# Optimization experiments

Measured on AMD Instinct MI355X. Metric: run time of the kernel, lower is better.

The kernel has to match this reference:

```python
import jax, jax.numpy as jnp
from jax import lax
import numpy as np

# Problem dims (see init_kwargs)
B, CIN, H, W = 4, 128, 128, 128
COUT, K, STRIDE, PAD, DIL, GROUPS, OG = 128, 3, 1, 1, 1, 1, 2


def setup_inputs() -> dict:
    key = jax.random.key(0)
    k0, k1, k2 = jax.random.split(key, 3)
    x = jax.random.normal(k0, (B, CIN, H, W), dtype=jnp.float32)
    off_ch = 3 * OG * K * K  # with_mask=True -> scale=3 (dy, dx, mask)
    # Small random offset-conv weights so offsets are non-trivial (zero-init would degenerate to plain conv)
    w_off = jax.random.normal(k1, (off_ch, CIN, K, K), dtype=jnp.float32) * 0.01
    b_off = jnp.zeros((off_ch,), jnp.float32)
    stdv = 1.0 / np.sqrt(CIN * K * K)
    weight = jax.random.uniform(k2, (COUT, CIN // GROUPS, K, K), jnp.float32, -stdv, stdv)
    bias = jnp.zeros((COUT,), jnp.float32)
    return {"x": x, "w_off": w_off, "b_off": b_off, "weight": weight, "bias": bias}


def _deform_conv2d(x, offset, mask, weight, bias):
    # x: [B,C,H,W]; offset: [B,2*OG*K2,Ho,Wo]; mask: [B,OG*K2,Ho,Wo]
    Bn, C, Hn, Wn = x.shape
    O = weight.shape[0]
    K2 = K * K
    Ho = (Hn + 2 * PAD - DIL * (K - 1) - 1) // STRIDE + 1
    Wo = (Wn + 2 * PAD - DIL * (K - 1) - 1) // STRIDE + 1
    # torchvision layout: per offset group, per kernel point, (dy, dx) interleaved
    off = offset.reshape(Bn, OG, K2, 2, Ho, Wo)
    kg = (jnp.arange(K) * DIL).astype(x.dtype)
    kyf = jnp.repeat(kg, K)  # [K2] kernel row offset, k2 = i*K + j
    kxf = jnp.tile(kg, K)    # [K2] kernel col offset
    base_y = (jnp.arange(Ho) * STRIDE - PAD).astype(x.dtype)
    base_x = (jnp.arange(Wo) * STRIDE - PAD).astype(x.dtype)
    # sampling coords: [B,OG,K2,Ho,Wo]
    sy = base_y[None, None, None, :, None] + kyf[None, None, :, None, None] + off[:, :, :, 0]
    sx = base_x[None, None, None, None, :] + kxf[None, None, :, None, None] + off[:, :, :, 1]
    y0f = jnp.floor(sy)
    x0f = jnp.floor(sx)
    ly = sy - y0f  # bilinear fractional weights
    lx = sx - x0f
    y0 = y0f.astype(jnp.int32)
    x0 = x0f.astype(jnp.int32)
    Cg = C // OG
    xg = x.reshape(Bn, OG, Cg, Hn * Wn)

    def gather(iy, ix):
        # zero-padding semantics: out-of-range corners contribute 0
        valid = ((iy >= 0) & (iy < Hn) & (ix >= 0) & (ix < Wn)).astype(x.dtype)
        idx = (jnp.clip(iy, 0, Hn - 1) * Wn + jnp.clip(ix, 0, Wn - 1)).reshape(Bn, OG, 1, -1)
        v = jnp.take_along_axis(xg, idx, axis=3).reshape(Bn, OG, Cg, K2, Ho, Wo)
        return v * valid[:, :, None]

    v00 = gather(y0, x0)
    v01 = gather(y0, x0 + 1)
    v10 = gather(y0 + 1, x0)
    v11 = gather(y0 + 1, x0 + 1)
    wy = ly[:, :, None]  # broadcast over channel dim
    wx = lx[:, :, None]
    val = (v00 * (1 - wy) * (1 - wx) + v01 * (1 - wy) * wx
           + v10 * wy * (1 - wx) + v11 * wy * wx)
    # modulated DCNv2: multiply sampled values by sigmoid mask
    val = val * mask.reshape(Bn, OG, 1, K2, Ho, Wo)
    # im2col GEMM: cols [B,G,(C/G)*K2,Ho*Wo] x weight [G,O/G,(C/G)*K2]
    cols = val.reshape(Bn, GROUPS, (C // GROUPS) * K2, Ho * Wo)
    wg = weight.reshape(GROUPS, O // GROUPS, (C // GROUPS) * K2)
    out = jnp.einsum('gok,bgkn->bgon', wg, cols).reshape(Bn, O, Ho, Wo)
    return out + bias[None, :, None, None]


def reference(x, w_off, b_off, weight, bias):
    off_out = lax.conv_general_dilated(
        x, w_off, (STRIDE, STRIDE), [(PAD, PAD), (PAD, PAD)],
        rhs_dilation=(DIL, DIL), dimension_numbers=('NCHW', 'OIHW', 'NCHW')
    ) + b_off[None, :, None, None]
    oh, ow, m = jnp.split(off_out, 3, axis=1)
    offset = jnp.concatenate([oh, ow], axis=1)
    mask = jax.nn.sigmoid(m)
    return _deform_conv2d(x, offset, mask, weight, bias)
```

## Files before the change

kernel.cpp:

```cpp
#include <hip/hip_runtime.h>
#include <math.h>

#define NB 4
#define NC 128
#define NH 128
#define NW 128
#define NHW (NH*NW)
#define NCOUT 128

#define SY_OFF 0
#define SX_OFF 1179648
#define MK_OFF 2359296
#define WOFF_OFF 3538944
#define WMAIN_OFF 3580416
#define XT_OFF 3663360

typedef short short8 __attribute__((ext_vector_type(8)));
typedef float f32x4 __attribute__((ext_vector_type(4)));

__device__ inline short f2bf(float f) {
    unsigned u = __float_as_uint(f);
    u = (u + 0x7FFFu + ((u >> 16) & 1u)) >> 16;
    return (short)u;
}
__device__ inline unsigned pack2(float lo, float hi) {
    unsigned r;
    asm("v_cvt_pk_bf16_f32 %0, %1, %2" : "=v"(r) : "v"(lo), "v"(hi));
    return r;
}
__device__ inline float bflo(unsigned u) { return __uint_as_float(u << 16); }
__device__ inline float bfhi(unsigned u) { return __uint_as_float(u & 0xffff0000u); }

__device__ inline void gload_lds16(const void* g, void* l) {
    __builtin_amdgcn_global_load_lds(
        (const __attribute__((address_space(1))) unsigned int*)g,
        (__attribute__((address_space(3))) unsigned int*)l, 16, 0, 0);
}

__global__ void wtrans_kernel(const float* __restrict__ w_off,
                              const float* __restrict__ weight,
                              float* __restrict__ ws)
{
    int i = blockIdx.x * 256 + threadIdx.x;
    if (i < 36*2304) {
        int s = i / 2304, rem = i - s*2304;
        int row = rem / 36, c = rem - row*36;
        int chunk = s / 9, k2 = s - 9*chunk;
        float v = (row < 54 && c < 32) ? w_off[(row*NC + chunk*32 + c)*9 + k2] : 0.f;
        ((short*)(ws + WOFF_OFF))[i] = f2bf(v);
    } else if (i < 36*2304 + 36*4608) {
        int j = i - 36*2304;
        int s = j / 4608, rem = j - s*4608;
        int row = rem / 36, c = rem - row*36;
        int chunk = s / 9, k2 = s - 9*chunk;
        float v = (c < 32) ? weight[(row*NC + chunk*32 + c)*9 + k2] : 0.f;
        ((short*)(ws + WMAIN_OFF))[j] = f2bf(v);
    }
}

__global__ __launch_bounds__(256) void xtrans_kernel(
    const float* __restrict__ x, float* __restrict__ ws)
{
    short* xT = (short*)(ws + XT_OFF);
    const int bid = blockIdx.x;
    const int ys = bid & 15, cg = (bid >> 4) & 15, b = bid >> 8;
    const int col = threadIdx.x & 127, rr = threadIdx.x >> 7;
    const float* xb = x + ((long)(b*NC + cg*8))*NHW;
#pragma unroll
    for (int yy = 0; yy < 4; ++yy) {
        const int y = ys*8 + yy*2 + rr;
        const float* p = xb + y*NW + col;
        float v[8];
#pragma unroll
        for (int q = 0; q < 8; ++q) v[q] = p[q*NHW];
        uint4 u = make_uint4(pack2(v[0],v[1]), pack2(v[2],v[3]),
                             pack2(v[4],v[5]), pack2(v[6],v[7]));
        *(uint4*)&xT[(((long)(b*16+cg)*NH + y)*NW + col)*8] = u;
    }
}

__global__ __launch_bounds__(512, 4) void offconv_kernel(
    float* __restrict__ ws, const float* __restrict__ b_off)
{
    __shared__ short wslab[2][2304];
    int bid = blockIdx.x;
    bid = (bid & 7) * 64 + (bid >> 3);
    const int b   = bid >> 7;
    const int ho  = bid & 127;
    const int tid = threadIdx.x;
    const int lane = tid & 63;
    const int wid = tid >> 6;
    const int n = lane & 15, g = lane >> 4;
    const int px = wid*16 + n;
    const short* woff = (const short*)(ws + WOFF_OFF);
    const char*  xTb  = (const char*)((const short*)(ws + XT_OFF) + (long)b*16*NHW*8);

    f32x4 acc[4];
#pragma unroll
    for (int rf = 0; rf < 4; ++rf) acc[rf] = (f32x4){0.f,0.f,0.f,0.f};

    auto DMA = [&](int it, int buf) {
        if (tid < 288) gload_lds16(woff + it*2304 + tid*8, &wslab[buf][tid*8]);
    };
    auto LOADB = [&](int it) -> short8 {
        const int chunk = it/9, k2 = it - 9*chunk;
        const int y = ho + k2/3 - 1, xc = px + (k2%3) - 1;
        short8 bf = (short8){0,0,0,0,0,0,0,0};
        if ((unsigned)y < NH && (unsigned)xc < NW)
            bf = *(const short8*)(xTb + ((long)(chunk*4 + g)*NHW + y*NW + xc)*16);
        return bf;
    };

    DMA(0, 0);
    short8 bcur = LOADB(0);
    __syncthreads();

#pragma unroll 1
    for (int it = 0; it < 36; ++it) {
        const int cur = it & 1, nxt = cur ^ 1;
        short8 bnext;
        if (it < 35) { DMA(it+1, nxt); bnext = LOADB(it+1); }
        __builtin_amdgcn_sched_barrier(0);
#pragma unroll
        for (int rf = 0; rf < 4; ++rf) {
            short8 af = *(const short8*)&wslab[cur][(rf*16 + n)*36 + 8*g];
            acc[rf] = __builtin_amdgcn_mfma_f32_16x16x32_bf16(af, bcur, acc[rf], 0,0,0);
        }
        __syncthreads();
        bcur = bnext;
    }

#pragma unroll
    for (int rf = 0; rf < 4; ++rf) {
#pragma unroll
        for (int r = 0; r < 4; ++r) {
            int cout = 16*rf + 4*g + r;
            if (cout >= 54) continue;
            float v = acc[rf][r] + b_off[cout];
            if (cout < 36) {
                int og = cout / 18, rem = cout - 18*og;
                int k2c = rem >> 1, d = cout & 1;
                float base = d ? (float)(px - 1 + (k2c % 3))
                              : (float)(ho - 1 + (k2c / 3));
                ws[(d ? SX_OFF : SY_OFF) + (((b*2+og)*9 + k2c)*NHW) + ho*NW + px] = v + base;
            } else {
                int cc = cout - 36;
                int og = cc / 9, k2c = cc - 9*og;
                ws[MK_OFF + (((b*2+og)*9 + k2c)*NHW) + ho*NW + px] = 1.f/(1.f+expf(-v));
            }
        }
    }
}

__global__ __launch_bounds__(512, 4) void deform_kernel(
    const float* __restrict__ ws_c, float* __restrict__ ws,
    const float* __restrict__ bias, float* __restrict__ out)
{
    __shared__ int4   pI[9][128];
    __shared__ float4 pW[9][128];
    __shared__ short  vals[2][128][40];
    __shared__ short  wslab[2][4608];

    int bid = blockIdx.x;
    bid = (bid & 7) * 64 + (bid >> 3);
    const int b   = bid >> 7;
    const int ho  = bid & 127;
    const int tid = threadIdx.x;
    const int lane = tid & 63;
    const int wid = tid >> 6;
    const int n = lane & 15, g = lane >> 4;
    const int ch  = wid & 1;
    const int pxq = wid >> 1;
    const int sp  = tid & 127;
    const int sub = tid >> 7;
    const short* wmn = (const short*)(ws + WMAIN_OFF);
    const char*  xTb = (const char*)((const short*)(ws + XT_OFF) + (long)b*16*NHW*8);

    f32x4 acc[4][2];
#pragma unroll
    for (int rf = 0; rf < 4; ++rf) {
        acc[rf][0] = (f32x4){0.f,0.f,0.f,0.f};
        acc[rf][1] = (f32x4){0.f,0.f,0.f,0.f};
    }

    auto DMA = [&](int slabIdx, int buf) {
        const short* src = wmn + slabIdx*4608;
        gload_lds16(src + tid*8, &wslab[buf][tid*8]);
        if (tid < 64) gload_lds16(src + 4096 + tid*8, &wslab[buf][4096 + tid*8]);
    };

    auto FIN = [&](const uint4& A, const uint4& Bc, const uint4& Cc, const uint4& D,
                   const float4& Wv, int buf) {
        uint4 u; unsigned* up = (unsigned*)&u;
        const unsigned* a = (const unsigned*)&A;
        const unsigned* bq = (const unsigned*)&Bc;
        const unsigned* c = (const unsigned*)&Cc;
        const unsigned* d = (const unsigned*)&D;
#pragma unroll
        for (int e = 0; e < 4; ++e) {
            float lo = Wv.x*bflo(a[e]) + Wv.y*bflo(bq[e]) + Wv.z*bflo(c[e]) + Wv.w*bflo(d[e]);
            float hi = Wv.x*bfhi(a[e]) + Wv.y*bfhi(bq[e]) + Wv.z*bfhi(c[e]) + Wv.w*bfhi(d[e]);
            up[e] = pack2(lo, hi);
        }
        *(uint4*)&vals[buf][sp][sub*8] = u;
    };

    DMA(0, 0);

#pragma unroll 1
    for (int og = 0; og < 2; ++og) {
        if (og) __syncthreads();
        for (int e = tid; e < 1152; e += 512) {
            const int k2 = e >> 7, px = e & 127;
            const int sidx = (((b*2+og)*9 + k2)*NHW) + ho*NW + px;
            const float sy = ws[SY_OFF + sidx];
            const float sx = ws[SX_OFF + sidx];
            const float m  = ws[MK_OFF + sidx];
            const float y0f = floorf(sy), x0f = floorf(sx);
            const float ly = sy - y0f, lx = sx - x0f;
            const int y0 = (int)y0f, x0i = (int)x0f;
            const int y1 = y0 + 1, x1 = x0i + 1;
            const bool vy0 = (unsigned)y0 < NH, vy1 = (unsigned)y1 < NH;
            const bool vx0 = (unsigned)x0i < NW, vx1 = (unsigned)x1 < NW;
            const int cy0 = min(max(y0,0),NH-1), cy1 = min(max(y1,0),NH-1);
            const int cx0 = min(max(x0i,0),NW-1), cx1 = min(max(x1,0),NW-1);
            pI[k2][px] = make_int4((cy0*NW + cx0)*16, (cy0*NW + cx1)*16,
                                   (cy1*NW + cx0)*16, (cy1*NW + cx1)*16);
            pW[k2][px] = make_float4(
                (vy0 && vx0) ? (1.f-ly)*(1.f-lx)*m : 0.f,
                (vy0 && vx1) ? (1.f-ly)*lx*m       : 0.f,
                (vy1 && vx0) ? ly*(1.f-lx)*m       : 0.f,
                (vy1 && vx1) ? ly*lx*m             : 0.f);
        }
        __syncthreads();

        const int it0 = og*18;

        {
            const int chunk = it0/9, k2n = it0 - 9*chunk;
            const int4  I  = pI[k2n][sp];
            const float4 Wv = pW[k2n][sp];
            const char* xp = xTb + (long)(chunk*4 + sub)*(NHW*16);
            uint4 A  = *(const uint4*)(xp + I.x);
            uint4 Bc = *(const uint4*)(xp + I.y);
            uint4 Cc = *(const uint4*)(xp + I.z);
            uint4 D  = *(const uint4*)(xp + I.w);
            FIN(A, Bc, Cc, D, Wv, 0);
        }
        __syncthreads();

#pragma unroll 1
        for (int it = it0; it < it0 + 18; ++it) {
            const int cur = it & 1, nxt = cur ^ 1;
            const bool pre = (it < it0 + 17);

            uint4 A, Bc, Cc, D;
            float4 Wv;
            if (pre) {
                const int itn = it + 1;
                const int chunk = itn/9, k2n = itn - 9*chunk;
                const int4 I = pI[k2n][sp];
                Wv = pW[k2n][sp];
                const char* xp = xTb + (long)(chunk*4 + sub)*(NHW*16);
                A  = *(const uint4*)(xp + I.x);
                Bc = *(const uint4*)(xp + I.y);
                Cc = *(const uint4*)(xp + I.z);
                D  = *(const uint4*)(xp + I.w);
                DMA(itn, nxt);
            } else if (og == 0) {
                DMA(18, nxt);
            }
            __builtin_amdgcn_sched_barrier(0);

            {
                short8 bf0 = *(const short8*)&vals[cur][pxq*32 + n][8*g];
                short8 bf1 = *(const short8*)&vals[cur][pxq*32 + 16 + n][8*g];
#pragma unroll
                for (int rf = 0; rf < 4; ++rf) {
                    short8 af = *(const short8*)&wslab[cur][(ch*64 + rf*16 + n)*36 + 8*g];
                    acc[rf][0] = __builtin_amdgcn_mfma_f32_16x16x32_bf16(af, bf0, acc[rf][0], 0,0,0);
                    acc[rf][1] = __builtin_amdgcn_mfma_f32_16x16x32_bf16(af, bf1, acc[rf][1], 0,0,0);
                }
            }
            __builtin_amdgcn_sched_barrier(0);

            if (pre) FIN(A, Bc, Cc, D, Wv, nxt);
            __syncthreads();
        }
    }

#pragma unroll
    for (int rf = 0; rf < 4; ++rf) {
#pragma unroll
        for (int pxb = 0; pxb < 2; ++pxb) {
            const int px = pxq*32 + pxb*16 + n;
#pragma unroll
            for (int r = 0; r < 4; ++r) {
                const int cout = ch*64 + rf*16 + 4*g + r;
                out[((b*NCOUT + cout)*NH + ho)*NW + px] = acc[rf][pxb][r] + bias[cout];
            }
        }
    }
}

extern "C" void kernel_launch(void* const* d_in, const int* in_sizes, int n_in,
                              void* d_out, int out_size, void* d_ws, size_t ws_size,
                              hipStream_t stream)
{
    const float* x      = (const float*)d_in[0];
    const float* w_off  = (const float*)d_in[1];
    const float* b_off  = (const float*)d_in[2];
    const float* weight = (const float*)d_in[3];
    const float* bias   = (const float*)d_in[4];
    float* out = (float*)d_out;
    float* ws  = (float*)d_ws;

    hipLaunchKernelGGL(wtrans_kernel, dim3(972), dim3(256), 0, stream,
                       w_off, weight, ws);
    hipLaunchKernelGGL(xtrans_kernel, dim3(1024), dim3(256), 0, stream,
                       x, ws);
    hipLaunchKernelGGL(offconv_kernel, dim3(NB*NH), dim3(512), 0, stream,
                       ws, b_off);
    hipLaunchKernelGGL(deform_kernel, dim3(NB*NH), dim3(512), 0, stream,
                       ws, ws, bias, out);
}
```

Baseline: 90.62 us.

## Split deform blocks to half-rows and load weight fragments directly into registers

The deform kernel now uses 256-thread blocks that each cover half an output row, doubling the grid. The LDS weight slab and its async DMA are removed; each wave loads its bf16 weight A-fragments straight from global memory into registers, prefetched one iteration ahead, and the weight layout drops its 36-wide padding to a dense 32. Sampling indices are stored as short4 to shrink LDS use. The aim is lower LDS footprint and higher occupancy, at the cost of redundant global weight loads per wave and duplicated per-pixel setup work across more blocks.

```diff
diff --git a/kernel.cpp b/kernel.cpp
--- a/kernel.cpp
+++ b/kernel.cpp
@@ -48,13 +48,12 @@
         int chunk = s / 9, k2 = s - 9*chunk;
         float v = (row < 54 && c < 32) ? w_off[(row*NC + chunk*32 + c)*9 + k2] : 0.f;
         ((short*)(ws + WOFF_OFF))[i] = f2bf(v);
-    } else if (i < 36*2304 + 36*4608) {
+    } else if (i < 36*2304 + 36*4096) {
         int j = i - 36*2304;
-        int s = j / 4608, rem = j - s*4608;
-        int row = rem / 36, c = rem - row*36;
+        int s = j >> 12, rem = j & 4095;
+        int row = rem >> 5, c = rem & 31;
         int chunk = s / 9, k2 = s - 9*chunk;
-        float v = (c < 32) ? weight[(row*NC + chunk*32 + c)*9 + k2] : 0.f;
-        ((short*)(ws + WMAIN_OFF))[j] = f2bf(v);
+        ((short*)(ws + WMAIN_OFF))[j] = f2bf(weight[(row*NC + chunk*32 + c)*9 + k2]);
     }
 }
 
@@ -152,27 +151,27 @@
     }
 }
 
-__global__ __launch_bounds__(512, 4) void deform_kernel(
+__global__ __launch_bounds__(256, 4) void deform_kernel(
     const float* __restrict__ ws_c, float* __restrict__ ws,
     const float* __restrict__ bias, float* __restrict__ out)
 {
-    __shared__ int4   pI[9][128];
-    __shared__ float4 pW[9][128];
-    __shared__ short  vals[2][128][40];
-    __shared__ short  wslab[2][4608];
+    __shared__ short4 pI[9][64];
+    __shared__ float4 pW[9][64];
+    __shared__ short  vals[2][64][40];
 
     int bid = blockIdx.x;
-    bid = (bid & 7) * 64 + (bid >> 3);
-    const int b   = bid >> 7;
-    const int ho  = bid & 127;
+    bid = (bid & 7) * 128 + (bid >> 3);
+    const int b   = bid >> 8;
+    const int ho  = (bid >> 1) & 127;
+    const int wb  = (bid & 1) * 64;
     const int tid = threadIdx.x;
     const int lane = tid & 63;
     const int wid = tid >> 6;
     const int n = lane & 15, g = lane >> 4;
     const int ch  = wid & 1;
-    const int pxq = wid >> 1;
-    const int sp  = tid & 127;
-    const int sub = tid >> 7;
+    const int pxh = wid >> 1;
+    const int sp  = tid & 63;
+    const int sub = tid >> 6;
     const short* wmn = (const short*)(ws + WMAIN_OFF);
     const char*  xTb = (const char*)((const short*)(ws + XT_OFF) + (long)b*16*NHW*8);
 
@@ -182,12 +181,6 @@
         acc[rf][0] = (f32x4){0.f,0.f,0.f,0.f};
         acc[rf][1] = (f32x4){0.f,0.f,0.f,0.f};
     }
-
-    auto DMA = [&](int slabIdx, int buf) {
-        const short* src = wmn + slabIdx*4608;
-        gload_lds16(src + tid*8, &wslab[buf][tid*8]);
-        if (tid < 64) gload_lds16(src + 4096 + tid*8, &wslab[buf][4096 + tid*8]);
-    };
 
     auto FIN = [&](const uint4& A, const uint4& Bc, const uint4& Cc, const uint4& D,
                    const float4& Wv, int buf) {
@@ -205,14 +198,17 @@
         *(uint4*)&vals[buf][sp][sub*8] = u;
     };
 
-    DMA(0, 0);
+    short8 acur0, acur1, acur2, acur3;
+    #define LOADA(dst, it, rf) \
+        dst = *(const short8*)(wmn + (it)*4096 + (ch*64 + (rf)*16 + n)*32 + 8*g)
 
 #pragma unroll 1
     for (int og = 0; og < 2; ++og) {
+        const int it0 = og*18;
         if (og) __syncthreads();
-        for (int e = tid; e < 1152; e += 512) {
-            const int k2 = e >> 7, px = e & 127;
-            const int sidx = (((b*2+og)*9 + k2)*NHW) + ho*NW + px;
+        for (int e = tid; e < 576; e += 256) {
+            const int k2 = e >> 6, px = e & 63;
+            const int sidx = (((b*2+og)*9 + k2)*NHW) + ho*NW + wb + px;
             const float sy = ws[SY_OFF + sidx];
             const float sx = ws[SX_OFF + sidx];
             const float m  = ws[MK_OFF + sidx];
@@ -224,8 +220,8 @@
             const bool vx0 = (unsigned)x0i < NW, vx1 = (unsigned)x1 < NW;
             const int cy0 = min(max(y0,0),NH-1), cy1 = min(max(y1,0),NH-1);
             const int cx0 = min(max(x0i,0),NW-1), cx1 = min(max(x1,0),NW-1);
-            pI[k2][px] = make_int4((cy0*NW + cx0)*16, (cy0*NW + cx1)*16,
-                                   (cy1*NW + cx0)*16, (cy1*NW + cx1)*16);
+            pI[k2][px] = make_short4((short)(cy0*NW + cx0), (short)(cy0*NW + cx1),
+                                     (short)(cy1*NW + cx0), (short)(cy1*NW + cx1));
             pW[k2][px] = make_float4(
                 (vy0 && vx0) ? (1.f-ly)*(1.f-lx)*m : 0.f,
                 (vy0 && vx1) ? (1.f-ly)*lx*m       : 0.f,
@@ -234,17 +230,19 @@
         }
         __syncthreads();
 
-        const int it0 = og*18;
-
+        if (og == 0) {
+            LOADA(acur0, 0, 0); LOADA(acur1, 0, 1);
+            LOADA(acur2, 0, 2); LOADA(acur3, 0, 3);
+        }
         {
             const int chunk = it0/9, k2n = it0 - 9*chunk;
-            const int4  I  = pI[k2n][sp];
+            const short4 I = pI[k2n][sp];
             const float4 Wv = pW[k2n][sp];
             const char* xp = xTb + (long)(chunk*4 + sub)*(NHW*16);
-            uint4 A  = *(const uint4*)(xp + I.x);
-            uint4 Bc = *(const uint4*)(xp + I.y);
-            uint4 Cc = *(const uint4*)(xp + I.z);
-            uint4 D  = *(const uint4*)(xp + I.w);
+            uint4 A  = *(const uint4*)(xp + (((int)I.x) << 4));
+            uint4 Bc = *(const uint4*)(xp + (((int)I.y) << 4));
+            uint4 Cc = *(const uint4*)(xp + (((int)I.z) << 4));
+            uint4 D  = *(const uint4*)(xp + (((int)I.w) << 4));
             FIN(A, Bc, Cc, D, Wv, 0);
         }
         __syncthreads();
@@ -254,38 +252,43 @@
             const int cur = it & 1, nxt = cur ^ 1;
             const bool pre = (it < it0 + 17);
 
+            short8 anxt0, anxt1, anxt2, anxt3;
             uint4 A, Bc, Cc, D;
             float4 Wv;
+            if (it < 35) {
+                LOADA(anxt0, it+1, 0); LOADA(anxt1, it+1, 1);
+                LOADA(anxt2, it+1, 2); LOADA(anxt3, it+1, 3);
+            }
             if (pre) {
                 const int itn = it + 1;
                 const int chunk = itn/9, k2n = itn - 9*chunk;
-                const int4 I = pI[k2n][sp];
+                const short4 I = pI[k2n][sp];
                 Wv = pW[k2n][sp];
                 const char* xp = xTb + (long)(chunk*4 + sub)*(NHW*16);
-                A  = *(const uint4*)(xp + I.x);
-                Bc = *(const uint4*)(xp + I.y);
-                Cc = *(const uint4*)(xp + I.z);
-                D  = *(const uint4*)(xp + I.w);
-                DMA(itn, nxt);
-            } else if (og == 0) {
-                DMA(18, nxt);
+                A  = *(const uint4*)(xp + (((int)I.x) << 4));
+                Bc = *(const uint4*)(xp + (((int)I.y) << 4));
+                Cc = *(const uint4*)(xp + (((int)I.z) << 4));
+                D  = *(const uint4*)(xp + (((int)I.w) << 4));
             }
             __builtin_amdgcn_sched_barrier(0);
 
             {
-                short8 bf0 = *(const short8*)&vals[cur][pxq*32 + n][8*g];
-                short8 bf1 = *(const short8*)&vals[cur][pxq*32 + 16 + n][8*g];
-#pragma unroll
-                for (int rf = 0; rf < 4; ++rf) {
-                    short8 af = *(const short8*)&wslab[cur][(ch*64 + rf*16 + n)*36 + 8*g];
-                    acc[rf][0] = __builtin_amdgcn_mfma_f32_16x16x32_bf16(af, bf0, acc[rf][0], 0,0,0);
-                    acc[rf][1] = __builtin_amdgcn_mfma_f32_16x16x32_bf16(af, bf1, acc[rf][1], 0,0,0);
-                }
+                short8 bf0 = *(const short8*)&vals[cur][pxh*32 + n][8*g];
+                short8 bf1 = *(const short8*)&vals[cur][pxh*32 + 16 + n][8*g];
+                acc[0][0] = __builtin_amdgcn_mfma_f32_16x16x32_bf16(acur0, bf0, acc[0][0], 0,0,0);
+                acc[0][1] = __builtin_amdgcn_mfma_f32_16x16x32_bf16(acur0, bf1, acc[0][1], 0,0,0);
+                acc[1][0] = __builtin_amdgcn_mfma_f32_16x16x32_bf16(acur1, bf0, acc[1][0], 0,0,0);
+                acc[1][1] = __builtin_amdgcn_mfma_f32_16x16x32_bf16(acur1, bf1, acc[1][1], 0,0,0);
+                acc[2][0] = __builtin_amdgcn_mfma_f32_16x16x32_bf16(acur2, bf0, acc[2][0], 0,0,0);
+                acc[2][1] = __builtin_amdgcn_mfma_f32_16x16x32_bf16(acur2, bf1, acc[2][1], 0,0,0);
+                acc[3][0] = __builtin_amdgcn_mfma_f32_16x16x32_bf16(acur3, bf0, acc[3][0], 0,0,0);
+                acc[3][1] = __builtin_amdgcn_mfma_f32_16x16x32_bf16(acur3, bf1, acc[3][1], 0,0,0);
             }
             __builtin_amdgcn_sched_barrier(0);
 
             if (pre) FIN(A, Bc, Cc, D, Wv, nxt);
             __syncthreads();
+            acur0 = anxt0; acur1 = anxt1; acur2 = anxt2; acur3 = anxt3;
         }
     }
 
@@ -293,7 +296,7 @@
     for (int rf = 0; rf < 4; ++rf) {
 #pragma unroll
         for (int pxb = 0; pxb < 2; ++pxb) {
-            const int px = pxq*32 + pxb*16 + n;
+            const int px = wb + pxh*32 + pxb*16 + n;
 #pragma unroll
             for (int r = 0; r < 4; ++r) {
                 const int cout = ch*64 + rf*16 + 4*g + r;
@@ -301,6 +304,7 @@
             }
         }
     }
+    #undef LOADA
 }
 
 extern "C" void kernel_launch(void* const* d_in, const int* in_sizes, int n_in,
@@ -315,12 +319,12 @@
     float* out = (float*)d_out;
     float* ws  = (float*)d_ws;
 
-    hipLaunchKernelGGL(wtrans_kernel, dim3(972), dim3(256), 0, stream,
+    hipLaunchKernelGGL(wtrans_kernel, dim3(900), dim3(256), 0, stream,
                        w_off, weight, ws);
     hipLaunchKernelGGL(xtrans_kernel, dim3(1024), dim3(256), 0, stream,
                        x, ws);
     hipLaunchKernelGGL(offconv_kernel, dim3(NB*NH), dim3(512), 0, stream,
                        ws, b_off);
-    hipLaunchKernelGGL(deform_kernel, dim3(NB*NH), dim3(512), 0, stream,
+    hipLaunchKernelGGL(deform_kernel, dim3(NB*NH*2), dim3(256), 0, stream,
                        ws, ws, bias, out);
 }
```

Measured after the change: 106.4 us. 1.17x slower.

## Deepen gather prefetch to two iterations and merge offset-group sampling setup

Applied to the files above, without the earlier changes.

Sampling indices and bilinear weights for both offset groups are now computed once up front into LDS. Indices are stored as 16-bit shorts and weights as packed fp16, which shrinks LDS enough to hold 18 rows. The main loop is unrolled by two with ping-pong register buffers, so the global gathers run two iterations ahead of the MFMA work. Barriers use explicit vmcnt/lgkmcnt waits instead of __syncthreads. This removes the mid-kernel stall between offset groups and hides gather latency, at the cost of more registers and fp16 rounding of the weights.

```diff
diff --git a/kernel.cpp b/kernel.cpp
--- a/kernel.cpp
+++ b/kernel.cpp
@@ -30,7 +30,14 @@
 }
 __device__ inline float bflo(unsigned u) { return __uint_as_float(u << 16); }
 __device__ inline float bfhi(unsigned u) { return __uint_as_float(u & 0xffff0000u); }
-
+__device__ inline unsigned pkf16(float a, float b) {
+    auto h = __builtin_amdgcn_cvt_pkrtz(a, b);
+    unsigned r; __builtin_memcpy(&r, &h, 4); return r;
+}
+__device__ inline float f16f(unsigned s) {
+    unsigned short us = (unsigned short)s;
+    __fp16 h; __builtin_memcpy(&h, &us, 2); return (float)h;
+}
 __device__ inline void gload_lds16(const void* g, void* l) {
     __builtin_amdgcn_global_load_lds(
         (const __attribute__((address_space(1))) unsigned int*)g,
@@ -156,8 +163,8 @@
     const float* __restrict__ ws_c, float* __restrict__ ws,
     const float* __restrict__ bias, float* __restrict__ out)
 {
-    __shared__ int4   pI[9][128];
-    __shared__ float4 pW[9][128];
+    __shared__ short4 pI[18][128];
+    __shared__ uint2  pWp[18][128];
     __shared__ short  vals[2][128][40];
     __shared__ short  wslab[2][4608];
 
@@ -188,18 +195,30 @@
         gload_lds16(src + tid*8, &wslab[buf][tid*8]);
         if (tid < 64) gload_lds16(src + 4096 + tid*8, &wslab[buf][4096 + tid*8]);
     };
-
-    auto FIN = [&](const uint4& A, const uint4& Bc, const uint4& Cc, const uint4& D,
-                   const float4& Wv, int buf) {
+    auto GLOAD = [&](int j, uint4* G) {
+        const int chunk = j/9;
+        const int row = (j/18)*9 + (j%9);
+        const short4 I = pI[row][sp];
+        const char* xp = xTb + (long)(chunk*4 + sub)*(NHW*16);
+        G[0] = *(const uint4*)(xp + (((int)I.x) << 4));
+        G[1] = *(const uint4*)(xp + (((int)I.y) << 4));
+        G[2] = *(const uint4*)(xp + (((int)I.z) << 4));
+        G[3] = *(const uint4*)(xp + (((int)I.w) << 4));
+    };
+    auto FIN = [&](int j, uint4* G, int buf) {
+        const int row = (j/18)*9 + (j%9);
+        const uint2 wp = *(const uint2*)&pWp[row][sp];
+        const float W0 = f16f(wp.x), W1 = f16f(wp.x >> 16);
+        const float W2 = f16f(wp.y), W3 = f16f(wp.y >> 16);
         uint4 u; unsigned* up = (unsigned*)&u;
-        const unsigned* a = (const unsigned*)&A;
-        const unsigned* bq = (const unsigned*)&Bc;
-        const unsigned* c = (const unsigned*)&Cc;
-        const unsigned* d = (const unsigned*)&D;
+        const unsigned* a = (const unsigned*)&G[0];
+        const unsigned* bq = (const unsigned*)&G[1];
+        const unsigned* c = (const unsigned*)&G[2];
+        const unsigned* d = (const unsigned*)&G[3];
 #pragma unroll
         for (int e = 0; e < 4; ++e) {
-            float lo = Wv.x*bflo(a[e]) + Wv.y*bflo(bq[e]) + Wv.z*bflo(c[e]) + Wv.w*bflo(d[e]);
-            float hi = Wv.x*bfhi(a[e]) + Wv.y*bfhi(bq[e]) + Wv.z*bfhi(c[e]) + Wv.w*bfhi(d[e]);
+            float lo = W0*bflo(a[e]) + W1*bflo(bq[e]) + W2*bflo(c[e]) + W3*bflo(d[e]);
+            float hi = W0*bfhi(a[e]) + W1*bfhi(bq[e]) + W2*bfhi(c[e]) + W3*bfhi(d[e]);
             up[e] = pack2(lo, hi);
         }
         *(uint4*)&vals[buf][sp][sub*8] = u;
@@ -207,86 +226,71 @@
 
     DMA(0, 0);
 
+    for (int e = tid; e < 2304; e += 512) {
+        const int og = e / 1152, rem = e - og*1152;
+        const int k2 = rem >> 7, px = rem & 127;
+        const int sidx = (((b*2+og)*9 + k2)*NHW) + ho*NW + px;
+        const float sy = ws[SY_OFF + sidx];
+        const float sx = ws[SX_OFF + sidx];
+        const float m  = ws[MK_OFF + sidx];
+        const float y0f = floorf(sy), x0f = floorf(sx);
+        const float ly = sy - y0f, lx = sx - x0f;
+        const int y0 = (int)y0f, x0i = (int)x0f;
+        const int y1 = y0 + 1, x1 = x0i + 1;
+        const bool vy0 = (unsigned)y0 < NH, vy1 = (unsigned)y1 < NH;
+        const bool vx0 = (unsigned)x0i < NW, vx1 = (unsigned)x1 < NW;
+        const int cy0 = min(max(y0,0),NH-1), cy1 = min(max(y1,0),NH-1);
+        const int cx0 = min(max(x0i,0),NW-1), cx1 = min(max(x1,0),NW-1);
+        pI[og*9+k2][px] = make_short4(
+            (short)(cy0*NW + cx0), (short)(cy0*NW + cx1),
+            (short)(cy1*NW + cx0), (short)(cy1*NW + cx1));
+        const float W0 = (vy0 && vx0) ? (1.f-ly)*(1.f-lx)*m : 0.f;
+        const float W1 = (vy0 && vx1) ? (1.f-ly)*lx*m       : 0.f;
+        const float W2 = (vy1 && vx0) ? ly*(1.f-lx)*m       : 0.f;
+        const float W3 = (vy1 && vx1) ? ly*lx*m             : 0.f;
+        pWp[og*9+k2][px] = make_uint2(pkf16(W0, W1), pkf16(W2, W3));
+    }
+    __syncthreads();
+
+    uint4 GA[4], GB[4];
+    GLOAD(0, GA);
+    FIN(0, GA, 0);
+    GLOAD(1, GB);
+    asm volatile("s_waitcnt lgkmcnt(0)" ::: "memory");
+    __builtin_amdgcn_s_barrier();
+    __builtin_amdgcn_sched_barrier(0);
+
+    auto BODY = [&](int it, uint4* Gfree, uint4* Gheld) {
+        const int cur = it & 1, nxt = cur ^ 1;
+        if (it < 35) DMA(it+1, nxt);
+        if (it < 34) GLOAD(it+2, Gfree);
+        __builtin_amdgcn_sched_barrier(0);
+        {
+            short8 bf0 = *(const short8*)&vals[cur][pxq*32 + n][8*g];
+            short8 bf1 = *(const short8*)&vals[cur][pxq*32 + 16 + n][8*g];
+#pragma unroll
+            for (int rf = 0; rf < 4; ++rf) {
+                short8 af = *(const short8*)&wslab[cur][(ch*64 + rf*16 + n)*36 + 8*g];
+                acc[rf][0] = __builtin_amdgcn_mfma_f32_16x16x32_bf16(af, bf0, acc[rf][0], 0,0,0);
+                acc[rf][1] = __builtin_amdgcn_mfma_f32_16x16x32_bf16(af, bf1, acc[rf][1], 0,0,0);
+            }
+        }
+        __builtin_amdgcn_sched_barrier(0);
+        if (it < 35) FIN(it+1, Gheld, nxt);
+        if (it < 34) {
+            asm volatile("s_waitcnt vmcnt(4) lgkmcnt(0)" ::: "memory");
+            __builtin_amdgcn_s_barrier();
+            __builtin_amdgcn_sched_barrier(0);
+        } else if (it == 34) {
+            asm volatile("s_waitcnt vmcnt(0) lgkmcnt(0)" ::: "memory");
+            __builtin_amdgcn_s_barrier();
+            __builtin_amdgcn_sched_barrier(0);
+        }
+    };
 #pragma unroll 1
-    for (int og = 0; og < 2; ++og) {
-        if (og) __syncthreads();
-        for (int e = tid; e < 1152; e += 512) {
-            const int k2 = e >> 7, px = e & 127;
-            const int sidx = (((b*2+og)*9 + k2)*NHW) + ho*NW + px;
-            const float sy = ws[SY_OFF + sidx];
-            const float sx = ws[SX_OFF + sidx];
-            const float m  = ws[MK_OFF + sidx];
-            const float y0f = floorf(sy), x0f = floorf(sx);
-            const float ly = sy - y0f, lx = sx - x0f;
-            const int y0 = (int)y0f, x0i = (int)x0f;
-            const int y1 = y0 + 1, x1 = x0i + 1;
-            const bool vy0 = (unsigned)y0 < NH, vy1 = (unsigned)y1 < NH;
-            const bool vx0 = (unsigned)x0i < NW, vx1 = (unsigned)x1 < NW;
-            const int cy0 = min(max(y0,0),NH-1), cy1 = min(max(y1,0),NH-1);
-            const int cx0 = min(max(x0i,0),NW-1), cx1 = min(max(x1,0),NW-1);
-            pI[k2][px] = make_int4((cy0*NW + cx0)*16, (cy0*NW + cx1)*16,
-                                   (cy1*NW + cx0)*16, (cy1*NW + cx1)*16);
-            pW[k2][px] = make_float4(
-                (vy0 && vx0) ? (1.f-ly)*(1.f-lx)*m : 0.f,
-                (vy0 && vx1) ? (1.f-ly)*lx*m       : 0.f,
-                (vy1 && vx0) ? ly*(1.f-lx)*m       : 0.f,
-                (vy1 && vx1) ? ly*lx*m             : 0.f);
-        }
-        __syncthreads();
-
-        const int it0 = og*18;
-
-        {
-            const int chunk = it0/9, k2n = it0 - 9*chunk;
-            const int4  I  = pI[k2n][sp];
-            const float4 Wv = pW[k2n][sp];
-            const char* xp = xTb + (long)(chunk*4 + sub)*(NHW*16);
-            uint4 A  = *(const uint4*)(xp + I.x);
-            uint4 Bc = *(const uint4*)(xp + I.y);
-            uint4 Cc = *(const uint4*)(xp + I.z);
-            uint4 D  = *(const uint4*)(xp + I.w);
-            FIN(A, Bc, Cc, D, Wv, 0);
-        }
-        __syncthreads();
-
-#pragma unroll 1
-        for (int it = it0; it < it0 + 18; ++it) {
-            const int cur = it & 1, nxt = cur ^ 1;
-            const bool pre = (it < it0 + 17);
-
-            uint4 A, Bc, Cc, D;
-            float4 Wv;
-            if (pre) {
-                const int itn = it + 1;
-                const int chunk = itn/9, k2n = itn - 9*chunk;
-                const int4 I = pI[k2n][sp];
-                Wv = pW[k2n][sp];
-                const char* xp = xTb + (long)(chunk*4 + sub)*(NHW*16);
-                A  = *(const uint4*)(xp + I.x);
-                Bc = *(const uint4*)(xp + I.y);
-                Cc = *(const uint4*)(xp + I.z);
-                D  = *(const uint4*)(xp + I.w);
-                DMA(itn, nxt);
-            } else if (og == 0) {
-                DMA(18, nxt);
-            }
-            __builtin_amdgcn_sched_barrier(0);
-
-            {
-                short8 bf0 = *(const short8*)&vals[cur][pxq*32 + n][8*g];
-                short8 bf1 = *(const short8*)&vals[cur][pxq*32 + 16 + n][8*g];
-#pragma unroll
-                for (int rf = 0; rf < 4; ++rf) {
-                    short8 af = *(const short8*)&wslab[cur][(ch*64 + rf*16 + n)*36 + 8*g];
-                    acc[rf][0] = __builtin_amdgcn_mfma_f32_16x16x32_bf16(af, bf0, acc[rf][0], 0,0,0);
-                    acc[rf][1] = __builtin_amdgcn_mfma_f32_16x16x32_bf16(af, bf1, acc[rf][1], 0,0,0);
-                }
-            }
-            __builtin_amdgcn_sched_barrier(0);
-
-            if (pre) FIN(A, Bc, Cc, D, Wv, nxt);
-            __syncthreads();
-        }
+    for (int t = 0; t < 18; ++t) {
+        BODY(2*t,     GA, GB);
+        BODY(2*t + 1, GB, GA);
     }
 
 #pragma unroll
```

Result: slower. 92.58 us (+2.2%).
